# Kernel tuning notes

Hardware: AMD Instinct MI355X
Metric: run time of the kernel (lower is better)

The kernel has to match this reference:

```python
import jax, jax.numpy as jnp
import numpy as np

B, S, K = 64, 2048, 256


def setup_inputs() -> dict:
    key = jax.random.key(0)
    k1, k2 = jax.random.split(key)
    inp = jax.random.normal(k1, (B, S, K), dtype=jnp.float32)
    # target probabilities: random nonnegative, normalized over classes
    raw = jax.random.uniform(k2, (B, S, K), dtype=jnp.float32)
    target = raw / jnp.sum(raw, axis=-1, keepdims=True)
    mask = jnp.ones((B, S), dtype=jnp.float32)
    return {"input": inp, "target": target, "mask": mask}


def reference(input, target, mask):
    # flatten: [B,S,K] -> [n,k], mask [B,S] -> [n]
    k = input.shape[-1]
    flat_in = input.reshape(-1, k)
    flat_targ = target.reshape(-1, k)
    flat_mask = mask.reshape(-1)
    # soft cross entropy: sum_y targ[:,y] * (-log_softmax(in)[:,y]) * mask
    # single log-softmax pass instead of the per-class loop
    log_p = jax.nn.log_softmax(flat_in, axis=-1)          # [n,k]
    per_tok = -jnp.sum(flat_targ * log_p, axis=-1)        # [n]
    cum_losses = per_tok * flat_mask                      # [n]
    return jnp.mean(cum_losses)                           # reduction='mean'
```

## Files before the change

### kernel.cpp

```cpp
#include <hip/hip_runtime.h>


using vfloat4 = __attribute__((ext_vector_type(4))) float;

struct Chunk {
    vfloat4 x[4];
    vfloat4 g[4];
    float   m[4];
};

__device__ __forceinline__ void load_chunk(const float* __restrict__ input,
                                           const float* __restrict__ target,
                                           const float* __restrict__ mask,
                                           int t0, int lane, Chunk& c)
{
    #pragma unroll
    for (int i = 0; i < 4; ++i) {
        c.x[i] = __builtin_nontemporal_load(
            &((const vfloat4*)(input  + (size_t)(t0 + i) * 256))[lane]);
        c.g[i] = __builtin_nontemporal_load(
            &((const vfloat4*)(target + (size_t)(t0 + i) * 256))[lane]);
        c.m[i] = mask[t0 + i];
    }
}

__device__ __forceinline__ void process_chunk(const Chunk& c,
                                              float& dot_acc, float& lse_acc)
{
    float se[4];
    #pragma unroll
    for (int i = 0; i < 4; ++i) {
        dot_acc += c.m[i] * (c.g[i].x * c.x[i].x + c.g[i].y * c.x[i].y
                           + c.g[i].z * c.x[i].z + c.g[i].w * c.x[i].w);
        se[i] = __expf(c.x[i].x) + __expf(c.x[i].y)
              + __expf(c.x[i].z) + __expf(c.x[i].w);
    }
    #pragma unroll
    for (int off = 32; off >= 1; off >>= 1) {
        #pragma unroll
        for (int i = 0; i < 4; ++i) se[i] += __shfl_xor(se[i], off, 64);
    }
    #pragma unroll
    for (int i = 0; i < 4; ++i) lse_acc += c.m[i] * __logf(se[i]);
}

__global__ __launch_bounds__(256) void sxent_partial_kernel(
    const float* __restrict__ input,
    const float* __restrict__ target,
    const float* __restrict__ mask,
    float* __restrict__ partials,
    int n_tokens)
{
    const int lane  = threadIdx.x & 63;
    const int wave  = threadIdx.x >> 6;
    const int wpb   = blockDim.x >> 6;
    const int gwave = blockIdx.x * wpb + wave;
    const int nwave = gridDim.x * wpb;

    float dot_acc = 0.0f;
    float lse_acc = 0.0f;

    const int stride = nwave * 4;
    int t = gwave * 4;

    if (t + 3 < n_tokens) {
        Chunk cur;
        load_chunk(input, target, mask, t, lane, cur);
        for (int tn = t + stride; tn + 3 < n_tokens; tn += stride) {
            Chunk nxt;
            load_chunk(input, target, mask, tn, lane, nxt);
            process_chunk(cur, dot_acc, lse_acc);
            cur = nxt;
        }
        process_chunk(cur, dot_acc, lse_acc);
    }

    #pragma unroll
    for (int off = 32; off >= 1; off >>= 1)
        dot_acc += __shfl_xor(dot_acc, off, 64);

    __shared__ float lds[4];
    if (lane == 0) lds[wave] = lse_acc - dot_acc;
    __syncthreads();
    if (threadIdx.x == 0) {
        float s = 0.0f;
        for (int w = 0; w < wpb; ++w) s += lds[w];
        partials[blockIdx.x] = s;
    }
}

__global__ __launch_bounds__(256) void sxent_final_kernel(
    const float* __restrict__ partials, int n_partials,
    float* __restrict__ out, float inv_n)
{
    float s = 0.0f;
    for (int i = threadIdx.x; i < n_partials; i += blockDim.x)
        s += partials[i];

    __shared__ float lds[256];
    lds[threadIdx.x] = s;
    __syncthreads();
    #pragma unroll
    for (int stride = 128; stride >= 1; stride >>= 1) {
        if (threadIdx.x < stride) lds[threadIdx.x] += lds[threadIdx.x + stride];
        __syncthreads();
    }
    if (threadIdx.x == 0) out[0] = lds[0] * inv_n;
}

extern "C" void kernel_launch(void* const* d_in, const int* in_sizes, int n_in,
                              void* d_out, int out_size, void* d_ws, size_t ws_size,
                              hipStream_t stream) {
    const float* input  = (const float*)d_in[0];
    const float* target = (const float*)d_in[1];
    const float* mask   = (const float*)d_in[2];
    float* out      = (float*)d_out;
    float* partials = (float*)d_ws;

    const int n_tokens = in_sizes[2];
    const int blocks   = 1024;

    sxent_partial_kernel<<<blocks, 256, 0, stream>>>(input, target, mask,
                                                     partials, n_tokens);
    sxent_final_kernel<<<1, 256, 0, stream>>>(partials, blocks, out,
                                              1.0f / (float)n_tokens);
}
```

Measured before the change: 251.9 us.

## Map 16 lanes per token and deepen prefetch to three stages

Each group of 16 lanes now handles one token, so a wave covers four tokens with a 16-lane shuffle reduction instead of four 64-lane reductions. Each lane reads four strided float4 segments of its token row. Prefetching goes from double to triple buffering to keep more loads in flight. The per-lane log-sum-exp is replicated 16 times and scaled by 1/16 at the end, which adds a reduction of lse across lanes and more registers per stage.

After: 254.0 us. About the same (+0.9%).

```diff
diff --git a/kernel.cpp b/kernel.cpp
--- a/kernel.cpp
+++ b/kernel.cpp
@@ -3,45 +3,46 @@
 
 using vfloat4 = __attribute__((ext_vector_type(4))) float;
 
-struct Chunk {
+struct Stage {
     vfloat4 x[4];
     vfloat4 g[4];
-    float   m[4];
+    float   m;
 };
 
-__device__ __forceinline__ void load_chunk(const float* __restrict__ input,
+__device__ __forceinline__ void load_stage(const float* __restrict__ input,
                                            const float* __restrict__ target,
                                            const float* __restrict__ mask,
-                                           int t0, int lane, Chunk& c)
+                                           int t0, int lane, Stage& s)
 {
+    const int tok = t0 + (lane >> 4);
+    const vfloat4* xr = (const vfloat4*)input  + (size_t)tok * 64 + (lane & 15);
+    const vfloat4* gr = (const vfloat4*)target + (size_t)tok * 64 + (lane & 15);
     #pragma unroll
-    for (int i = 0; i < 4; ++i) {
-        c.x[i] = __builtin_nontemporal_load(
-            &((const vfloat4*)(input  + (size_t)(t0 + i) * 256))[lane]);
-        c.g[i] = __builtin_nontemporal_load(
-            &((const vfloat4*)(target + (size_t)(t0 + i) * 256))[lane]);
-        c.m[i] = mask[t0 + i];
+    for (int j = 0; j < 4; ++j) {
+        s.x[j] = __builtin_nontemporal_load(xr + 16 * j);
+        s.g[j] = __builtin_nontemporal_load(gr + 16 * j);
     }
+    s.m = mask[tok];
 }
 
-__device__ __forceinline__ void process_chunk(const Chunk& c,
+__device__ __forceinline__ void process_stage(const Stage& s,
                                               float& dot_acc, float& lse_acc)
 {
-    float se[4];
+    float se = 0.0f, dp = 0.0f;
     #pragma unroll
-    for (int i = 0; i < 4; ++i) {
-        dot_acc += c.m[i] * (c.g[i].x * c.x[i].x + c.g[i].y * c.x[i].y
-                           + c.g[i].z * c.x[i].z + c.g[i].w * c.x[i].w);
-        se[i] = __expf(c.x[i].x) + __expf(c.x[i].y)
-              + __expf(c.x[i].z) + __expf(c.x[i].w);
+    for (int j = 0; j < 4; ++j) {
+        se += __expf(s.x[j].x) + __expf(s.x[j].y)
+            + __expf(s.x[j].z) + __expf(s.x[j].w);
+        dp += s.g[j].x * s.x[j].x + s.g[j].y * s.x[j].y
+            + s.g[j].z * s.x[j].z + s.g[j].w * s.x[j].w;
     }
+    dot_acc += s.m * dp;
+
     #pragma unroll
-    for (int off = 32; off >= 1; off >>= 1) {
-        #pragma unroll
-        for (int i = 0; i < 4; ++i) se[i] += __shfl_xor(se[i], off, 64);
-    }
-    #pragma unroll
-    for (int i = 0; i < 4; ++i) lse_acc += c.m[i] * __logf(se[i]);
+    for (int off = 8; off >= 1; off >>= 1)
+        se += __shfl_xor(se, off, 64);
+
+    lse_acc += s.m * __logf(se);
 }
 
 __global__ __launch_bounds__(256) void sxent_partial_kernel(
@@ -61,26 +62,33 @@
     float lse_acc = 0.0f;
 
     const int stride = nwave * 4;
-    int t = gwave * 4;
 
-    if (t + 3 < n_tokens) {
-        Chunk cur;
-        load_chunk(input, target, mask, t, lane, cur);
-        for (int tn = t + stride; tn + 3 < n_tokens; tn += stride) {
-            Chunk nxt;
-            load_chunk(input, target, mask, tn, lane, nxt);
-            process_chunk(cur, dot_acc, lse_acc);
-            cur = nxt;
-        }
-        process_chunk(cur, dot_acc, lse_acc);
+    Stage s0, s1, s2;
+    int  t0 = gwave * 4;
+    bool v0 = (t0 + 3) < n_tokens;
+    if (v0) load_stage(input, target, mask, t0, lane, s0);
+    int  t1 = t0 + stride;
+    bool v1 = (t1 + 3) < n_tokens;
+    if (v1) load_stage(input, target, mask, t1, lane, s1);
+
+    while (v0) {
+        const int  t2 = t1 + stride;
+        const bool v2 = (t2 + 3) < n_tokens;
+        if (v2) load_stage(input, target, mask, t2, lane, s2);
+        process_stage(s0, dot_acc, lse_acc);
+        s0 = s1; v0 = v1;
+        s1 = s2; v1 = v2;
+        t1 = t2;
     }
 
     #pragma unroll
-    for (int off = 32; off >= 1; off >>= 1)
+    for (int off = 32; off >= 1; off >>= 1) {
         dot_acc += __shfl_xor(dot_acc, off, 64);
+        lse_acc += __shfl_xor(lse_acc, off, 64);
+    }
 
     __shared__ float lds[4];
-    if (lane == 0) lds[wave] = lse_acc - dot_acc;
+    if (lane == 0) lds[wave] = lse_acc * 0.0625f - dot_acc;
     __syncthreads();
     if (threadIdx.x == 0) {
         float s = 0.0f;
```
